# Optimization experiments

Hardware: AMD Instinct MI355X
Metric: run time of the kernel (lower is better)

Reference implementation:

```python
import jax, jax.numpy as jnp
import numpy as np

B, NQ, NC, DC, DY = 4, 4096, 4096, 2, 8


def setup_inputs() -> dict:
    key = jax.random.key(0)
    k1, k2, k3 = jax.random.split(key, 3)
    x_query = jax.random.normal(k1, (B, NQ, DC), dtype=jnp.float32)
    x_context = jax.random.normal(k2, (B, NC, DC), dtype=jnp.float32)
    y_context = jax.random.normal(k3, (B, NC, DY), dtype=jnp.float32)
    log_length_scale = jnp.asarray(np.log(0.1), dtype=jnp.float32)
    return {
        "x_query": x_query,
        "x_context": x_context,
        "y_context": y_context,
        "log_length_scale": log_length_scale,
    }


def reference(x_query, x_context, y_context, log_length_scale):
    # Squared Euclidean distances: (B, NQ, NC).
    # cdist followed by .pow(2) == squared distance, so compute d2 directly.
    diff = x_query[:, :, None, :] - x_context[:, None, :, :]  # (B,NQ,NC,DC)
    d2 = jnp.sum(diff * diff, axis=-1)                         # (B,NQ,NC)
    length_scale = jnp.exp(log_length_scale)
    weights = jnp.exp(-d2 / (2.0 * length_scale ** 2))         # RBF kernel
    density = jnp.sum(weights, axis=-1, keepdims=True)         # (B,NQ,1)
    weights_norm = weights / (density + 1e-8)
    y_query = jnp.einsum('bqc,bcd->bqd', weights_norm, y_context)  # (B,NQ,DY)
    return jnp.concatenate([y_query, density], axis=-1)        # (B,NQ,DY+1)
```

## Files before the change

kernel.cpp:

```cpp
#include <hip/hip_runtime.h>


#define BB 4
#define NQ 4096
#define NC 4096
#define DY 8
#define NBQ (BB * NQ)

#if __has_builtin(__builtin_amdgcn_exp2f)
#define EXP2F(x) __builtin_amdgcn_exp2f(x)
#else
#define EXP2F(x) exp2f(x)
#endif

typedef short bf16x8 __attribute__((ext_vector_type(8)));
typedef float f32x4  __attribute__((ext_vector_type(4)));
typedef float f32x2  __attribute__((ext_vector_type(2)));

__device__ __forceinline__ short f2bf(float v) {
    return (short)(__builtin_bit_cast(unsigned, v) >> 16);
}
__device__ __forceinline__ unsigned fbits(float v) {
    return __builtin_bit_cast(unsigned, v);
}
__device__ __forceinline__ unsigned bfpair(float w0, float w1) {
#if __has_builtin(__builtin_amdgcn_perm)
    return __builtin_amdgcn_perm(fbits(w1), fbits(w0), 0x07060302u);
#else
    return (fbits(w1) & 0xFFFF0000u) | (fbits(w0) >> 16);
#endif
}

#define GSPLIT 8
#define CCHUNK (NC / GSPLIT)
#define NPAIR (CCHUNK / 2)
#define KSTEPS (CCHUNK / 32)
#define QPB 128
#define QB (NBQ / QPB)
#define JS ((size_t)GSPLIT * NBQ)
#define WS_FLOATS ((size_t)(DY + 1) * GSPLIT * NBQ)

__global__ __launch_bounds__(256, 4) void setconv_accum_mfma(
    const float* __restrict__ xq, const float* __restrict__ xc,
    const float* __restrict__ yc, const float* __restrict__ lls,
    float* __restrict__ ws)
{
    __shared__ float4 sxp[NPAIR];
    __shared__ float2 shp[NPAIR];
    __shared__ unsigned short yfrag[CCHUNK / 8][16][8];

    const int bid  = blockIdx.x;
    const int gs   = bid & (GSPLIT - 1);
    const int qb   = bid >> 3;
    const int b    = qb >> 5;
    const int tid  = threadIdx.x;
    const int lane = tid & 63;
    const int wv   = tid >> 6;
    const int m    = lane & 15;
    const int quad = lane >> 4;

    const float L    = lls[0];
    const float negk = -0.72134752044448f * EXP2F(L * -2.8853900817779268f);

    {
        const float4* xcp = (const float4*)(((const float2*)xc) + (size_t)b * NC + gs * CCHUNK);
        const float4 v = xcp[tid];
        sxp[tid] = make_float4(v.x, v.z, v.y, v.w);
        shp[tid] = make_float2(negk * fmaf(v.x, v.x, v.y * v.y),
                               negk * fmaf(v.z, v.z, v.w * v.w));
    }
    {
        const float4* yp = (const float4*)(yc + ((size_t)b * NC + gs * CCHUNK) * DY);
#pragma unroll
        for (int i = 0; i < 2; ++i) {
            const int c = tid + 256 * i;
            const float4 A  = yp[2 * c + 0];
            const float4 Bv = yp[2 * c + 1];
            const int g = c >> 3, j = c & 7;
            unsigned short* dst = &yfrag[g][0][j];
            dst[0 * 8] = (unsigned short)f2bf(A.x);
            dst[1 * 8] = (unsigned short)f2bf(A.y);
            dst[2 * 8] = (unsigned short)f2bf(A.z);
            dst[3 * 8] = (unsigned short)f2bf(A.w);
            dst[4 * 8] = (unsigned short)f2bf(Bv.x);
            dst[5 * 8] = (unsigned short)f2bf(Bv.y);
            dst[6 * 8] = (unsigned short)f2bf(Bv.z);
            dst[7 * 8] = (unsigned short)f2bf(Bv.w);
        }
        unsigned* yf32 = (unsigned*)yfrag;
#pragma unroll
        for (int i = 0; i < 8; ++i) {
            const int v = tid + 256 * i;
            const int g = v >> 5, r = v & 31;
            yf32[g * 64 + 32 + r] = (r < 4) ? 0x3F803F80u : 0u;
        }
    }

    f32x2 A0[2], A1[2], A2[2];
#pragma unroll
    for (int t = 0; t < 2; ++t) {
        const int q = qb * QPB + (wv * 2 + t) * 16 + m;
        const float2 qv = ((const float2*)xq)[q];
        const float a0 = negk * fmaf(qv.x, qv.x, qv.y * qv.y);
        const float a1 = -2.f * negk * qv.x;
        const float a2 = -2.f * negk * qv.y;
        A0[t] = (f32x2){a0, a0};
        A1[t] = (f32x2){a1, a1};
        A2[t] = (f32x2){a2, a2};
    }

    f32x4 acc0 = {0.f, 0.f, 0.f, 0.f};
    f32x4 acc1 = {0.f, 0.f, 0.f, 0.f};

    __syncthreads();

#pragma unroll 2
    for (int s = 0; s < KSTEPS; ++s) {
        const bf16x8 bfrag = *(const bf16x8*)&yfrag[s * 4 + quad][m][0];
        unsigned au0[4], au1[4];
#pragma unroll
        for (int jp = 0; jp < 4; ++jp) {
            const int P = s * 16 + quad * 4 + jp;
            const float4 xp = sxp[P];
            const float2 hp = shp[P];
            const f32x2 cx2 = {xp.x, xp.y};
            const f32x2 cy2 = {xp.z, xp.w};
            const f32x2 hc2 = {hp.x, hp.y};
            f32x2 t0 = __builtin_elementwise_fma(cx2, A1[0], hc2 + A0[0]);
            t0 = __builtin_elementwise_fma(cy2, A2[0], t0);
            f32x2 t1 = __builtin_elementwise_fma(cx2, A1[1], hc2 + A0[1]);
            t1 = __builtin_elementwise_fma(cy2, A2[1], t1);
            au0[jp] = bfpair(EXP2F(t0.x), EXP2F(t0.y));
            au1[jp] = bfpair(EXP2F(t1.x), EXP2F(t1.y));
        }
        const bf16x8 af0 = __builtin_bit_cast(bf16x8, *(uint4*)au0);
        const bf16x8 af1 = __builtin_bit_cast(bf16x8, *(uint4*)au1);
        acc0 = __builtin_amdgcn_mfma_f32_16x16x32_bf16(af0, bfrag, acc0, 0, 0, 0);
        acc1 = __builtin_amdgcn_mfma_f32_16x16x32_bf16(af1, bfrag, acc1, 0, 0, 0);
    }

    if (m <= 8) {
        const size_t base = (size_t)m * JS + (size_t)gs * NBQ + (size_t)qb * QPB;
#pragma unroll
        for (int r = 0; r < 4; ++r) {
            ws[base + (wv * 2 + 0) * 16 + quad * 4 + r] = acc0[r];
            ws[base + (wv * 2 + 1) * 16 + quad * 4 + r] = acc1[r];
        }
    }
}

__global__ __launch_bounds__(256) void setconv_reduce(
    const float* __restrict__ ws, float* __restrict__ out)
{
    __shared__ float part[4][64][DY + 1];
    const int tid  = threadIdx.x;
    const int qi   = tid & 63;
    const int sg   = tid >> 6;
    const int base = blockIdx.x * 64;
    const int bq   = base + qi;

#pragma unroll
    for (int j = 0; j < DY + 1; ++j) {
        float s = 0.f;
#pragma unroll
        for (int k = 0; k < GSPLIT / 4; ++k) {
            const int split = sg * (GSPLIT / 4) + k;
            s += ws[(size_t)j * JS + (size_t)split * NBQ + bq];
        }
        part[sg][qi][j] = s;
    }
    __syncthreads();

    for (int it = tid; it < 64 * (DY + 1); it += 256) {
        const int q2 = it / (DY + 1);
        const int j  = it - q2 * (DY + 1);
        const float den = part[0][q2][DY] + part[1][q2][DY] +
                          part[2][q2][DY] + part[3][q2][DY];
        float v;
        if (j == DY) {
            v = den;
        } else {
            const float s = part[0][q2][j] + part[1][q2][j] +
                            part[2][q2][j] + part[3][q2][j];
            v = s / (den + 1e-8f);
        }
        out[(size_t)base * (DY + 1) + it] = v;
    }
}

#define FSPLIT 8
#define FCCH (NC / FSPLIT)

__global__ __launch_bounds__(256) void setconv_zero(float4* __restrict__ out) {
    out[blockIdx.x * 256 + threadIdx.x] = make_float4(0.f, 0.f, 0.f, 0.f);
}

__global__ __launch_bounds__(256) void setconv_accum_atomic(
    const float* __restrict__ xq, const float* __restrict__ xc,
    const float* __restrict__ yc, const float* __restrict__ lls,
    float* __restrict__ out)
{
    const int bid   = blockIdx.x;
    const int split = bid & (FSPLIT - 1);
    const int qblk  = (bid / FSPLIT) & (NQ / 256 - 1);
    const int b     = bid / (FSPLIT * (NQ / 256));
    const int q     = qblk * 256 + threadIdx.x;

    const float L    = lls[0];
    const float negk = -0.72134752044448f * EXP2F(L * -2.8853900817779268f);

    const float2 qv = ((const float2*)xq)[b * NQ + q];
    const float qx0 = qv.x, qy0 = qv.y;

    float acc[DY], den = 0.f;
#pragma unroll
    for (int j = 0; j < DY; ++j) acc[j] = 0.f;

    const float2* __restrict__ xcp = ((const float2*)xc) + (size_t)b * NC;
    const float4* __restrict__ ycp = ((const float4*)yc) + (size_t)b * NC * 2;

    const int c0 = split * FCCH;
#pragma unroll 4
    for (int c = c0; c < c0 + FCCH; ++c) {
        const float2 cv = xcp[c];
        const float4 y0 = ycp[2 * c + 0];
        const float4 y1 = ycp[2 * c + 1];
        const float dx = qx0 - cv.x;
        const float dy = qy0 - cv.y;
        const float d2 = fmaf(dy, dy, dx * dx);
        const float w  = EXP2F(d2 * negk);
        den += w;
        acc[0] = fmaf(w, y0.x, acc[0]);
        acc[1] = fmaf(w, y0.y, acc[1]);
        acc[2] = fmaf(w, y0.z, acc[2]);
        acc[3] = fmaf(w, y0.w, acc[3]);
        acc[4] = fmaf(w, y1.x, acc[4]);
        acc[5] = fmaf(w, y1.y, acc[5]);
        acc[6] = fmaf(w, y1.z, acc[6]);
        acc[7] = fmaf(w, y1.w, acc[7]);
    }

    float* o = out + (size_t)(b * NQ + q) * (DY + 1);
#pragma unroll
    for (int j = 0; j < DY; ++j) atomicAdd(o + j, acc[j]);
    atomicAdd(o + DY, den);
}

__global__ __launch_bounds__(256) void setconv_norm(float* __restrict__ out) {
    const int q = blockIdx.x * 256 + threadIdx.x;
    float* o = out + (size_t)q * (DY + 1);
    const float inv = 1.0f / (o[DY] + 1e-8f);
#pragma unroll
    for (int j = 0; j < DY; ++j) o[j] *= inv;
}

extern "C" void kernel_launch(void* const* d_in, const int* in_sizes, int n_in,
                              void* d_out, int out_size, void* d_ws, size_t ws_size,
                              hipStream_t stream) {
    const float* xq  = (const float*)d_in[0];
    const float* xc  = (const float*)d_in[1];
    const float* yc  = (const float*)d_in[2];
    const float* lls = (const float*)d_in[3];
    float* out = (float*)d_out;

    if (ws_size >= WS_FLOATS * sizeof(float)) {
        float* ws = (float*)d_ws;
        setconv_accum_mfma<<<QB * GSPLIT, 256, 0, stream>>>(xq, xc, yc, lls, ws);
        setconv_reduce<<<NBQ / 64, 256, 0, stream>>>(ws, out);
    } else {
        setconv_zero<<<(NBQ * (DY + 1)) / 1024, 256, 0, stream>>>((float4*)out);
        setconv_accum_atomic<<<BB * (NQ / 256) * FSPLIT, 256, 0, stream>>>(xq, xc, yc, lls, out);
        setconv_norm<<<NBQ / 256, 256, 0, stream>>>(out);
    }
}
```

Before: 73.62 us.

## Split context steps across waves and reuse context loads over all query tiles

Each wave previously owned two 16-query tiles and swept the whole context chunk. Now each wave owns a quarter of the context steps and computes all eight query tiles, so every context load from shared memory and every y fragment is reused across eight MFMAs. Partial accumulators are then reduced across waves through shared memory, which adds several barriers and raises register pressure (eight accumulators plus per-tile coefficients). The output stores also become float4 writes.

```diff
diff --git a/kernel.cpp b/kernel.cpp
--- a/kernel.cpp
+++ b/kernel.cpp
@@ -36,6 +36,8 @@
 #define NPAIR (CCHUNK / 2)
 #define KSTEPS (CCHUNK / 32)
 #define QPB 128
+#define NT 8
+#define KPW (KSTEPS / 4)
 #define QB (NBQ / QPB)
 #define JS ((size_t)GSPLIT * NBQ)
 #define WS_FLOATS ((size_t)(DY + 1) * GSPLIT * NBQ)
@@ -47,7 +49,8 @@
 {
     __shared__ float4 sxp[NPAIR];
     __shared__ float2 shp[NPAIR];
-    __shared__ unsigned short yfrag[CCHUNK / 8][16][8];
+    __shared__ __attribute__((aligned(16)))
+        unsigned short yfrag[CCHUNK / 8][16][8];
 
     const int bid  = blockIdx.x;
     const int gs   = bid & (GSPLIT - 1);
@@ -96,56 +99,77 @@
         }
     }
 
-    f32x2 A0[2], A1[2], A2[2];
-#pragma unroll
-    for (int t = 0; t < 2; ++t) {
-        const int q = qb * QPB + (wv * 2 + t) * 16 + m;
+    float A0s[NT], A1s[NT], A2s[NT];
+#pragma unroll
+    for (int t = 0; t < NT; ++t) {
+        const int q = qb * QPB + t * 16 + m;
         const float2 qv = ((const float2*)xq)[q];
-        const float a0 = negk * fmaf(qv.x, qv.x, qv.y * qv.y);
-        const float a1 = -2.f * negk * qv.x;
-        const float a2 = -2.f * negk * qv.y;
-        A0[t] = (f32x2){a0, a0};
-        A1[t] = (f32x2){a1, a1};
-        A2[t] = (f32x2){a2, a2};
-    }
-
-    f32x4 acc0 = {0.f, 0.f, 0.f, 0.f};
-    f32x4 acc1 = {0.f, 0.f, 0.f, 0.f};
+        A0s[t] = negk * fmaf(qv.x, qv.x, qv.y * qv.y);
+        A1s[t] = -2.f * negk * qv.x;
+        A2s[t] = -2.f * negk * qv.y;
+    }
+
+    f32x4 acc[NT];
+#pragma unroll
+    for (int t = 0; t < NT; ++t) acc[t] = (f32x4){0.f, 0.f, 0.f, 0.f};
 
     __syncthreads();
 
-#pragma unroll 2
-    for (int s = 0; s < KSTEPS; ++s) {
+    for (int ks = 0; ks < KPW; ++ks) {
+        const int s = wv * KPW + ks;
         const bf16x8 bfrag = *(const bf16x8*)&yfrag[s * 4 + quad][m][0];
-        unsigned au0[4], au1[4];
+        float4 xp[4]; float2 hp[4];
 #pragma unroll
         for (int jp = 0; jp < 4; ++jp) {
             const int P = s * 16 + quad * 4 + jp;
-            const float4 xp = sxp[P];
-            const float2 hp = shp[P];
-            const f32x2 cx2 = {xp.x, xp.y};
-            const f32x2 cy2 = {xp.z, xp.w};
-            const f32x2 hc2 = {hp.x, hp.y};
-            f32x2 t0 = __builtin_elementwise_fma(cx2, A1[0], hc2 + A0[0]);
-            t0 = __builtin_elementwise_fma(cy2, A2[0], t0);
-            f32x2 t1 = __builtin_elementwise_fma(cx2, A1[1], hc2 + A0[1]);
-            t1 = __builtin_elementwise_fma(cy2, A2[1], t1);
-            au0[jp] = bfpair(EXP2F(t0.x), EXP2F(t0.y));
-            au1[jp] = bfpair(EXP2F(t1.x), EXP2F(t1.y));
-        }
-        const bf16x8 af0 = __builtin_bit_cast(bf16x8, *(uint4*)au0);
-        const bf16x8 af1 = __builtin_bit_cast(bf16x8, *(uint4*)au1);
-        acc0 = __builtin_amdgcn_mfma_f32_16x16x32_bf16(af0, bfrag, acc0, 0, 0, 0);
-        acc1 = __builtin_amdgcn_mfma_f32_16x16x32_bf16(af1, bfrag, acc1, 0, 0, 0);
-    }
-
-    if (m <= 8) {
-        const size_t base = (size_t)m * JS + (size_t)gs * NBQ + (size_t)qb * QPB;
-#pragma unroll
-        for (int r = 0; r < 4; ++r) {
-            ws[base + (wv * 2 + 0) * 16 + quad * 4 + r] = acc0[r];
-            ws[base + (wv * 2 + 1) * 16 + quad * 4 + r] = acc1[r];
-        }
+            xp[jp] = sxp[P];
+            hp[jp] = shp[P];
+        }
+#pragma unroll
+        for (int t = 0; t < NT; ++t) {
+            const f32x2 a0 = {A0s[t], A0s[t]};
+            const f32x2 a1 = {A1s[t], A1s[t]};
+            const f32x2 a2 = {A2s[t], A2s[t]};
+            unsigned au[4];
+#pragma unroll
+            for (int jp = 0; jp < 4; ++jp) {
+                const f32x2 cx2 = {xp[jp].x, xp[jp].y};
+                const f32x2 cy2 = {xp[jp].z, xp[jp].w};
+                const f32x2 hc2 = {hp[jp].x, hp[jp].y};
+                f32x2 tt = __builtin_elementwise_fma(cx2, a1, hc2 + a0);
+                tt = __builtin_elementwise_fma(cy2, a2, tt);
+                au[jp] = bfpair(EXP2F(tt.x), EXP2F(tt.y));
+            }
+            const bf16x8 af = __builtin_bit_cast(bf16x8, *(uint4*)au);
+            acc[t] = __builtin_amdgcn_mfma_f32_16x16x32_bf16(af, bfrag, acc[t], 0, 0, 0);
+        }
+    }
+
+    __syncthreads();
+    float4* rb = (float4*)&yfrag[0][0][0];
+    for (int h = 0; h < 4; ++h) {
+#pragma unroll
+        for (int u = 0; u < 2; ++u) {
+            const int t = h * 2 + u;
+            rb[(u * 4 + wv) * 64 + lane] =
+                make_float4(acc[t][0], acc[t][1], acc[t][2], acc[t][3]);
+        }
+        __syncthreads();
+        if (wv == h && m <= 8) {
+#pragma unroll
+            for (int u = 0; u < 2; ++u) {
+                const int t = h * 2 + u;
+                float4 v = rb[(u * 4 + 0) * 64 + lane];
+#pragma unroll
+                for (int w = 1; w < 4; ++w) {
+                    const float4 z = rb[(u * 4 + w) * 64 + lane];
+                    v.x += z.x; v.y += z.y; v.z += z.z; v.w += z.w;
+                }
+                *(float4*)&ws[(size_t)m * JS + (size_t)gs * NBQ +
+                              (size_t)qb * QPB + t * 16 + quad * 4] = v;
+            }
+        }
+        __syncthreads();
     }
 }
 
```

After: 73.85 us. Within noise of the previous version (+0.3%).
